# Kernel optimization log

Measured on AMD Instinct MI355X. Metric: run time of the kernel, lower is better.

The kernel has to match this reference:

```python
import jax, jax.numpy as jnp
import numpy as np
from jax import lax

# Constants (canonical show-attend-tell values)
ENCODER_DIM = 2048
ATTENTION_DIM = 512
DECODER_DIM = 512
EMBED_DIM = 512
VOCAB = 10000
B, L, T = 64, 196, 32


def setup_inputs() -> dict:
    key = jax.random.key(0)
    ks = jax.random.split(key, 20)
    s = 0.02
    inp = {
        "encoder_out": jax.random.normal(ks[0], (B, L, ENCODER_DIM), jnp.float32),
        "captions": jax.random.randint(ks[1], (B, T), 0, VOCAB),
        "lengths": jax.random.randint(ks[2], (B,), 2, T + 1).at[0].set(T),
        # parameters (stored as [in, out] for x @ W)
        "emb_table": jax.random.normal(ks[3], (VOCAB, EMBED_DIM), jnp.float32) * s,
        "W_a": jax.random.normal(ks[4], (ENCODER_DIM, ATTENTION_DIM), jnp.float32) * s,
        "U_a": jax.random.normal(ks[5], (DECODER_DIM, ATTENTION_DIM), jnp.float32) * s,
        "w_att": jax.random.normal(ks[6], (ATTENTION_DIM,), jnp.float32) * s,
        "fb_W": jax.random.normal(ks[7], (DECODER_DIM, 1), jnp.float32) * s,
        "fb_b": jnp.zeros((1,), jnp.float32),
        "W_ih": jax.random.normal(ks[8], (4 * DECODER_DIM, EMBED_DIM + ENCODER_DIM), jnp.float32) * s,
        "W_hh": jax.random.normal(ks[9], (4 * DECODER_DIM, DECODER_DIM), jnp.float32) * s,
        "b_ih": jnp.zeros((4 * DECODER_DIM,), jnp.float32),
        "b_hh": jnp.zeros((4 * DECODER_DIM,), jnp.float32),
        "fc_W": jax.random.normal(ks[10], (DECODER_DIM, VOCAB), jnp.float32) * s,
        "fc_b": jnp.zeros((VOCAB,), jnp.float32),
        "ih_W": jax.random.normal(ks[11], (ENCODER_DIM, DECODER_DIM), jnp.float32) * s,
        "ih_b": jnp.zeros((DECODER_DIM,), jnp.float32),
        "ic_W": jax.random.normal(ks[12], (ENCODER_DIM, DECODER_DIM), jnp.float32) * s,
        "ic_b": jnp.zeros((DECODER_DIM,), jnp.float32),
    }
    return inp


def reference(encoder_out, captions, lengths, emb_table, W_a, U_a, w_att,
              fb_W, fb_b, W_ih, W_hh, b_ih, b_hh, fc_W, fc_b,
              ih_W, ih_b, ic_W, ic_b):
    # sort by descending length (as in original)
    sort_idx = jnp.argsort(-lengths)
    enc = encoder_out[sort_idx]          # [B, L, D_enc]
    caps = captions[sort_idx]            # [B, T]
    dl = lengths[sort_idx] - 1           # decode lengths, max == T-1 by construction
    max_t = caps.shape[1] - 1

    emb = emb_table[caps]                # [B, T, E]
    mean = enc.mean(axis=1)
    h0 = jnp.tanh(mean @ ih_W + ih_b)    # [B, H]
    c0 = jnp.tanh(mean @ ic_W + ic_b)

    Wa_enc = enc @ W_a                   # [B, L, A], precomputed once

    def step(carry, xs):
        h, c = carry
        e_t, mask = xs                   # [B, E], [B] bool (dl > t)
        att = jnp.tanh(Wa_enc + (h @ U_a)[:, None, :])        # [B, L, A]
        energy = jnp.einsum('bla,a->bl', att, w_att)          # [B, L]
        alpha = jax.nn.softmax(energy, axis=1)
        context = jnp.einsum('bl,ble->be', alpha, enc)        # [B, D_enc]
        beta = jax.nn.sigmoid(h @ fb_W + fb_b)                # [B, 1]
        context = beta * context
        x = jnp.concatenate([e_t, context], axis=1)           # [B, E+D_enc]
        gates = x @ W_ih.T + b_ih + h @ W_hh.T + b_hh         # [B, 4H]
        i, f, g, o = jnp.split(gates, 4, axis=1)
        i = jax.nn.sigmoid(i); f = jax.nn.sigmoid(f)
        g = jnp.tanh(g); o = jax.nn.sigmoid(o)
        c_new = f * c + i * g
        h_new = o * jnp.tanh(c_new)
        m = mask[:, None]
        h2 = jnp.where(m, h_new, h)
        c2 = jnp.where(m, c_new, c)
        pred = jnp.where(m, h_new @ fc_W + fc_b, 0.0)         # [B, V]
        a_out = jnp.where(m, alpha, 0.0)
        return (h2, c2), (pred, a_out)

    xs = (emb[:, :max_t].transpose(1, 0, 2),                  # [T-1, B, E]
          jnp.arange(max_t)[:, None] < dl[None, :])           # [T-1, B]
    _, (preds, alphas) = lax.scan(step, (h0, c0), xs)
    predictions = preds.transpose(1, 0, 2)                    # [B, T-1, V]
    alphas = alphas.transpose(1, 0, 2)                        # [B, T-1, L]
    return predictions, caps, dl, alphas, sort_idx
```

## Files before the change

### kernel.cpp

```cpp
#include <hip/hip_runtime.h>
#include <cstdint>
#include <cstddef>

#define BB 64
#define LL 196
#define EE 2048
#define AD 512
#define DD 512
#define EM 512
#define VV 10000
#define TTOK 32
#define MT 31
#define KX 3072
#define G4 2048
#define VPAD 10048

#define OUT_PRED 0
#define OUT_CAPS (BB*MT*VV)
#define OUT_DL   (OUT_CAPS + BB*TTOK)
#define OUT_ALPH (OUT_DL + BB)
#define OUT_SIDX (OUT_ALPH + BB*MT*LL)

#define OFF_SIDX 0
#define OFF_DL   64
#define OFF_MEAN 128
#define OFF_C    (OFF_MEAN + BB*EE)
#define OFF_HU   (OFF_C + BB*DD)
#define OFF_ATT  (OFF_HU + BB*AD)
#define OFF_GACC (OFF_ATT + BB*256)
#define OFF_HB   (OFF_GACC + BB*G4)
#define OFF_XFB  (OFF_HB + BB*DD/2)
#define OFF_WB   (OFF_XFB + BB*KX/2)
#define OFF_FCWB (OFF_WB + (size_t)G4*KX/2)
#define OFF_UAB  (OFF_FCWB + (size_t)VPAD*DD/2)
#define OFF_WAB  (OFF_UAB + (size_t)AD*DD/2)
#define OFF_WAEB (OFF_WAB + (size_t)AD*EE/2)
#define OFF_EBF  (OFF_WAEB + (size_t)BB*LL*AD/2)
#define OFF_MEANB OFF_WAEB
#define OFF_IHB  (OFF_WAEB + 65536)
#define OFF_ICB  (OFF_WAEB + 65536 + 524288)

typedef unsigned short u16;
typedef __attribute__((ext_vector_type(8))) short bf16x8;
typedef __attribute__((ext_vector_type(4))) float f32x4;
#define MFMA16(a,b,c) __builtin_amdgcn_mfma_f32_16x16x32_bf16(a,b,c,0,0,0)

__device__ inline u16 f2bf(float x){
    unsigned u = __float_as_uint(x);
    unsigned r = (u + 0x7FFFu + ((u >> 16) & 1u)) >> 16;
    return (u16)r;
}
__device__ inline float bf2f(u16 x){ return __uint_as_float(((unsigned)x) << 16); }
__device__ inline float sigm(float x){ return 1.0f/(1.0f + __expf(-x)); }
__device__ inline float ftanh(float x){ return 2.0f/(1.0f + __expf(-2.0f*x)) - 1.0f; }

__device__ inline void gload16(const u16* g, u16* l){
    __builtin_amdgcn_global_load_lds((const __attribute__((address_space(1))) void*)g,
                                     (__attribute__((address_space(3))) void*)l, 16, 0, 0);
}

__global__ void k_sort(const int* __restrict__ lengths, const int* __restrict__ captions,
                       float* __restrict__ out, int* __restrict__ sidx, int* __restrict__ dl){
    __shared__ int len_s[BB];
    __shared__ int pos_s[BB];
    int i = threadIdx.x;
    len_s[i] = lengths[i];
    __syncthreads();
    int li = len_s[i];
    int rank = 0;
    for (int j = 0; j < BB; j++){
        int lj = len_s[j];
        rank += (lj > li) || (lj == li && j < i);
    }
    pos_s[rank] = i;
    __syncthreads();
    int src = pos_s[i];
    sidx[i] = src;
    int d = len_s[src] - 1;
    dl[i] = d;
    out[OUT_SIDX + i] = (float)src;
    out[OUT_DL + i]   = (float)d;
    for (int t = 0; t < TTOK; t++)
        out[OUT_CAPS + i*TTOK + t] = (float)captions[src*TTOK + t];
}

__global__ void k_ginit(float* __restrict__ gacc, float* __restrict__ mean){
    int gid = blockIdx.x*256 + threadIdx.x;
    if (gid < 65536) gacc[gid] = 0.f;
    else mean[gid - 65536] = 0.f;
}

__global__ void k_meanbf(const float* __restrict__ enc, const int* __restrict__ sidx,
                         float* __restrict__ mean, u16* __restrict__ ebf){
    int b = blockIdx.y;
    int e = (blockIdx.x*256 + threadIdx.x)*4;
    int l0 = blockIdx.z*98, l1 = l0 + 98;
    int src = sidx[b];
    const float* p = enc + (size_t)src*LL*EE + e;
    u16* o = ebf + (size_t)b*LL*EE + e;
    float sx = 0.f, sy = 0.f, sz = 0.f, sw = 0.f;
    for (int l = l0; l < l1; l++){
        float4 v = *(const float4*)(p + (size_t)l*EE);
        sx += v.x; sy += v.y; sz += v.z; sw += v.w;
        unsigned lo = (unsigned)f2bf(v.x) | ((unsigned)f2bf(v.y) << 16);
        unsigned hi = (unsigned)f2bf(v.z) | ((unsigned)f2bf(v.w) << 16);
        uint2 pk; pk.x = lo; pk.y = hi;
        *(uint2*)(o + (size_t)l*EE) = pk;
    }
    atomicAdd(&mean[b*EE + e + 0], sx);
    atomicAdd(&mean[b*EE + e + 1], sy);
    atomicAdd(&mean[b*EE + e + 2], sz);
    atomicAdd(&mean[b*EE + e + 3], sw);
}

__global__ void k_meanb(const float* __restrict__ mean, u16* __restrict__ meanb){
    int i = (blockIdx.x*256 + threadIdx.x)*8;
    float4 a = *(const float4*)(mean + i);
    float4 b = *(const float4*)(mean + i + 4);
// ... 43 lines not shown
    f32x4 acc[4] = {zz,zz,zz,zz};
    #pragma unroll 4
    for (int kc = 0; kc < 16; kc++){
        bf16x8 bv = *(const bf16x8*)(bp + kc*32);
        bf16x8 a0 = *(const bf16x8*)(ap + kc*32);
        bf16x8 a1 = *(const bf16x8*)(ap + 16*EE + kc*32);
        bf16x8 a2 = *(const bf16x8*)(ap + 32*EE + kc*32);
        bf16x8 a3 = *(const bf16x8*)(ap + 48*EE + kc*32);
        acc[0] = MFMA16(a0, bv, acc[0]);
        acc[1] = MFMA16(a1, bv, acc[1]);
        acc[2] = MFMA16(a2, bv, acc[2]);
        acc[3] = MFMA16(a3, bv, acc[3]);
    }
    int j = n0 + lane15;
    #pragma unroll
    for (int mt = 0; mt < 4; mt++)
        #pragma unroll
        for (int r = 0; r < 4; r++){
            int m = mt*16 + quad*4 + r;
            atomicAdd(&hc[z*32768 + m*512 + j], acc[mt][r]);
        }
}

__global__ void k_h0c0f(float* __restrict__ gacc, const float* __restrict__ ih_b,
                        const float* __restrict__ ic_b, const float* __restrict__ b_ih,
                        const float* __restrict__ b_hh, u16* __restrict__ hb,
                        float* __restrict__ c, u16* __restrict__ xfb){
    int gid = blockIdx.x*256 + threadIdx.x;
    if (gid < 65536){
        int z = gid >> 15;
        int mj = gid & 32767;
        int m = mj >> 9, j = mj & 511;
        float v = tanhf(gacc[gid] + (z ? ic_b[j] : ih_b[j]));
        if (z == 0){
            u16 hv = f2bf(v);
            hb[m*DD + j] = hv;
            xfb[(size_t)m*KX + 2560 + j] = hv;
        } else {
            c[m*DD + j] = v;
        }
    }
    int jj = gid & (G4-1);
    gacc[gid] = b_ih[jj] + b_hh[jj];
}

#define BKK 64
__global__ __launch_bounds__(256) void k_waenc2(const u16* __restrict__ ebf,
                                                const u16* __restrict__ Wab,
                                                u16* __restrict__ Waeb){
    __shared__ __align__(16) u16 As[2][128*BKK];
    __shared__ __align__(16) u16 Bs[2][128*BKK];
    int tid = threadIdx.x, lane = tid & 63, w = tid >> 6;
    int lane15 = lane & 15, quad = lane >> 4;
    int m0 = blockIdx.x * 128;
    int n0 = blockIdx.y * 128;

    int srow = w*8 + (lane >> 3);
    int scol = 8 * ((lane & 7) ^ (lane >> 3));
    const u16* ag = ebf + (size_t)(m0 + srow)*EE + scol;
    const u16* bg = Wab + (size_t)(n0 + srow)*EE + scol;

    f32x4 zz = {0.f,0.f,0.f,0.f};
    f32x4 acc[4][4];
    #pragma unroll
    for (int mt = 0; mt < 4; mt++)
        #pragma unroll
        for (int nt = 0; nt < 4; nt++) acc[mt][nt] = zz;

    int ar  = (w >> 1) * 64;
    int brr = (w & 1) * 64;
    int rx  = (lane15 & 7) << 3;

    {
        u16* la = &As[0][w*512 + lane*8];
        u16* lb = &Bs[0][w*512 + lane*8];
        #pragma unroll
        for (int i = 0; i < 4; i++){
            gload16(ag + (size_t)(i*32)*EE, la + i*2048);
            gload16(bg + (size_t)(i*32)*EE, lb + i*2048);
        }
    }
    __syncthreads();

    int cur = 0;
    for (int kt = 0; kt < 32; kt++){
        if (kt < 31){
            u16* la = &As[cur^1][w*512 + lane*8];
            u16* lb = &Bs[cur^1][w*512 + lane*8];
            const u16* a = ag + (size_t)(kt+1)*BKK;
            const u16* b = bg + (size_t)(kt+1)*BKK;
            #pragma unroll
            for (int i = 0; i < 4; i++){
                gload16(a + (size_t)(i*32)*EE, la + i*2048);
                gload16(b + (size_t)(i*32)*EE, lb + i*2048);
            }
        }
        bf16x8 af[4][2], bfr[4][2];
        #pragma unroll
        for (int mt = 0; mt < 4; mt++)
            #pragma unroll
            for (int ks = 0; ks < 2; ks++){
                af[mt][ks]  = *(const bf16x8*)&As[cur][(ar  + mt*16 + lane15)*BKK + ((ks*32 + quad*8) ^ rx)];
                bfr[mt][ks] = *(const bf16x8*)&Bs[cur][(brr + mt*16 + lane15)*BKK + ((ks*32 + quad*8) ^ rx)];
            }
        #pragma unroll
        for (int ks = 0; ks < 2; ks++)
            #pragma unroll
            for (int mt = 0; mt < 4; mt++)
                #pragma unroll
                for (int nt = 0; nt < 4; nt++)
                    acc[mt][nt] = MFMA16(af[mt][ks], bfr[nt][ks], acc[mt][nt]);
        __syncthreads();
        cur ^= 1;
    }

    #pragma unroll
    for (int mt = 0; mt < 4; mt++)
        #pragma unroll
        for (int nt = 0; nt < 4; nt++)
            #pragma unroll
            for (int r = 0; r < 4; r++){
                int row = m0 + ar + mt*16 + quad*4 + r;
                Waeb[(size_t)row*AD + n0 + brr + nt*16 + lane15] = f2bf(acc[mt][nt][r]);
            }
}

__global__ __launch_bounds__(256) void k_energyA(const u16* __restrict__ Waeb,
                       const float* __restrict__ hU, const float* __restrict__ w_att,
                       float* __restrict__ en){
    int tid = threadIdx.x, lane = tid & 63, w = tid >> 6;
    int b = blockIdx.x >> 2, sub = blockIdx.x & 3;

    const float* hub = hU + (size_t)b*AD;
    float hw[8], ww[8];
    #pragma unroll
    for (int ii = 0; ii < 8; ii++){
        hw[ii] = hub[ii*64 + lane];
        ww[ii] = w_att[ii*64 + lane];
    }
    int l0 = sub*49;
    for (int l = l0 + w; l < l0 + 49; l += 4){
        const u16* wa = Waeb + ((size_t)b*LL + l)*AD;
        float acc = 0.f;
        #pragma unroll
        for (int ii = 0; ii < 8; ii++)
            acc += ftanh(bf2f(wa[ii*64 + lane]) + hw[ii]) * ww[ii];
        #pragma unroll
        for (int off = 32; off; off >>= 1) acc += __shfl_xor(acc, off, 64);
        if (lane == 0) en[b*256 + l] = acc;
    }
}

__global__ __launch_bounds__(256) void k_ctx(const float* __restrict__ en,
                      const u16* __restrict__ ebf, const u16* __restrict__ hb,
                      const float* __restrict__ fb_W, const float* __restrict__ fb_b,
                      const float* __restrict__ emb_table, const int* __restrict__ captions,
                      const int* __restrict__ sidx, const int* __restrict__ dl,
                      u16* __restrict__ xfb, float* __restrict__ out, int t){
    __shared__ float red[256];
    __shared__ float alpha_s[LL];
    __shared__ float sbeta;
    int b = blockIdx.y, q = blockIdx.x, tid = threadIdx.x;

    float e = (tid < LL) ? en[b*256 + tid] : -3.0e38f;
    red[tid] = e; __syncthreads();
    for (int s = 128; s > 0; s >>= 1){ if (tid < s) red[tid] = fmaxf(red[tid], red[tid+s]); __syncthreads(); }
    float mx = red[0]; __syncthreads();
    float p = (tid < LL) ? __expf(e - mx) : 0.f;
    red[tid] = p; __syncthreads();
    for (int s = 128; s > 0; s >>= 1){ if (tid < s) red[tid] += red[tid+s]; __syncthreads(); }
    float ssum = red[0]; __syncthreads();
    float alpha = p / ssum;
    if (tid < LL){
        alpha_s[tid] = alpha;
        if (q == 0)
            out[OUT_ALPH + ((size_t)b*MT + t)*LL + tid] = (t < dl[b]) ? alpha : 0.f;
    }

    red[tid] = bf2f(hb[b*DD + tid]) * fb_W[tid]
             + bf2f(hb[b*DD + 256 + tid]) * fb_W[256 + tid];
    __syncthreads();
    for (int s = 128; s > 0; s >>= 1){ if (tid < s) red[tid] += red[tid+s]; __syncthreads(); }
    if (tid == 0) sbeta = sigm(red[0] + fb_b[0]);

    int cap = captions[sidx[b]*TTOK + t];
    if (tid < 128)
        xfb[(size_t)b*KX + q*128 + tid] = f2bf(emb_table[(size_t)cap*EM + q*128 + tid]);
    __syncthreads();

    float beta = sbeta;
    int e0 = q*512 + tid*2;
    const u16* pe = ebf + (size_t)b*LL*EE + e0;
    float ax = 0.f, ay = 0.f;
    for (int l = 0; l < LL; l++){
        unsigned u = *(const unsigned*)(pe + (size_t)l*EE);
        float a = alpha_s[l];
        ax += a * __uint_as_float(u << 16);
        ay += a * __uint_as_float(u & 0xFFFF0000u);
    }
    unsigned pk = (unsigned)f2bf(beta*ax) | ((unsigned)f2bf(beta*ay) << 16);
    *(unsigned*)(xfb + (size_t)b*KX + EM + e0) = pk;
}

__global__ void k_gates(const u16* __restrict__ Wb, const u16* __restrict__ xfb,
                        float* __restrict__ gacc){
    int tid = threadIdx.x, lane = tid & 63, w = tid >> 6;
    int lane15 = lane & 15, quad = lane >> 4;
    int n0 = blockIdx.x*64 + w*16;
    int kbase = blockIdx.y*384;
    const u16* bp = Wb + (size_t)(n0 + lane15)*KX + kbase + quad*8;
    const u16* ap = xfb + (size_t)lane15*KX + kbase + quad*8;
    f32x4 z = {0.f,0.f,0.f,0.f};
    f32x4 acc[4] = {z,z,z,z};
    #pragma unroll 4
    for (int kc = 0; kc < 12; kc++){
        bf16x8 bv = *(const bf16x8*)(bp + kc*32);
        bf16x8 a0 = *(const bf16x8*)(ap + kc*32);
        bf16x8 a1 = *(const bf16x8*)(ap + 16*KX + kc*32);
        bf16x8 a2 = *(const bf16x8*)(ap + 32*KX + kc*32);
        bf16x8 a3 = *(const bf16x8*)(ap + 48*KX + kc*32);
        acc[0] = MFMA16(a0, bv, acc[0]);
        acc[1] = MFMA16(a1, bv, acc[1]);
        acc[2] = MFMA16(a2, bv, acc[2]);
        acc[3] = MFMA16(a3, bv, acc[3]);
    }
    #pragma unroll
    for (int mt = 0; mt < 4; mt++)
        #pragma unroll
        for (int r = 0; r < 4; r++){
            int m = mt*16 + quad*4 + r;
            atomicAdd(&gacc[(size_t)m*G4 + n0 + lane15], acc[mt][r]);
        }
}

__global__ void k_update(float* __restrict__ gacc, const float* __restrict__ b_ih,
                         const float* __restrict__ b_hh, const int* __restrict__ dl,
                         u16* __restrict__ hb, float* __restrict__ c,
                         u16* __restrict__ xfb, int t){
    int gid = blockIdx.x*256 + threadIdx.x;
    int b = gid >> 9, d = gid & 511;
    size_t base = (size_t)b*G4 + d;
    float gi = gacc[base];
    float gf = gacc[base + 512];
    float gg = gacc[base + 1024];
    float go = gacc[base + 1536];
    float ig = sigm(gi), fg = sigm(gf), g = ftanh(gg), o = sigm(go);
    float cold = c[gid];
    float cn = fg*cold + ig*g;
    float hn = o*ftanh(cn);
    if (t < dl[b]){
        c[gid] = cn;
        u16 hv = f2bf(hn);
        hb[gid] = hv;
        xfb[(size_t)b*KX + 2560 + d] = hv;
    }
    gacc[base]        = b_ih[d]        + b_hh[d];
    gacc[base + 512]  = b_ih[d + 512]  + b_hh[d + 512];
    gacc[base + 1024] = b_ih[d + 1024] + b_hh[d + 1024];
    gacc[base + 1536] = b_ih[d + 1536] + b_hh[d + 1536];
}

__global__ void k_pred(const u16* __restrict__ fcWb, const float* __restrict__ fc_b,
                       const u16* __restrict__ Uab, const u16* __restrict__ hb,
                       const int* __restrict__ dl, float* __restrict__ out,
                       float* __restrict__ hU, int t, int hu_only){
    int tid = threadIdx.x, lane = tid & 63, w = tid >> 6;
    int lane15 = lane & 15, quad = lane >> 4;
    int bid = blockIdx.x;
    bool pred; int jc;
    if (hu_only){ pred = false; jc = bid; }
    else if (bid < 157){ pred = true; jc = bid; }
    else { pred = false; jc = bid - 157; }
    const u16* W = pred ? fcWb : Uab;
    int n0 = jc*64 + w*16;
    const u16* bp = W + (size_t)(n0 + lane15)*AD + quad*8;
    const u16* ap = hb + (size_t)lane15*AD + quad*8;
    f32x4 z = {0.f,0.f,0.f,0.f};
    f32x4 acc[4] = {z,z,z,z};
    #pragma unroll 4
    for (int kc = 0; kc < 16; kc++){
        bf16x8 bv = *(const bf16x8*)(bp + kc*32);
        bf16x8 a0 = *(const bf16x8*)(ap + kc*32);
        bf16x8 a1 = *(const bf16x8*)(ap + 16*AD + kc*32);
        bf16x8 a2 = *(const bf16x8*)(ap + 32*AD + kc*32);
        bf16x8 a3 = *(const bf16x8*)(ap + 48*AD + kc*32);
        acc[0] = MFMA16(a0, bv, acc[0]);
        acc[1] = MFMA16(a1, bv, acc[1]);
        acc[2] = MFMA16(a2, bv, acc[2]);
        acc[3] = MFMA16(a3, bv, acc[3]);
    }
    if (pred){
        int j = n0 + lane15;
        if (j < VV){
            float bias = fc_b[j];
            #pragma unroll
            for (int mt = 0; mt < 4; mt++)
                #pragma unroll
                for (int r = 0; r < 4; r++){
                    int b = mt*16 + quad*4 + r;
                    bool mk = t < dl[b];
                    out[OUT_PRED + ((size_t)b*MT + t)*VV + j] = mk ? acc[mt][r] + bias : 0.f;
                }
        }
    } else {
        int n = n0 + lane15;
        #pragma unroll
        for (int mt = 0; mt < 4; mt++)
            #pragma unroll
            for (int r = 0; r < 4; r++){
                int b = mt*16 + quad*4 + r;
                hU[(size_t)b*AD + n] = acc[mt][r];
            }
    }
}

extern "C" void kernel_launch(void* const* d_in, const int* in_sizes, int n_in,
                              void* d_out, int out_size, void* d_ws, size_t ws_size,
                              hipStream_t stream) {
    const float* enc       = (const float*)d_in[0];
    const int*   captions  = (const int*)d_in[1];
    const int*   lengths   = (const int*)d_in[2];
    const float* emb_table = (const float*)d_in[3];
    const float* W_a       = (const float*)d_in[4];
    const float* U_a       = (const float*)d_in[5];
    const float* w_att     = (const float*)d_in[6];
    const float* fb_W      = (const float*)d_in[7];
    const float* fb_b      = (const float*)d_in[8];
    const float* W_ih      = (const float*)d_in[9];
    const float* W_hh      = (const float*)d_in[10];
    const float* b_ih      = (const float*)d_in[11];
    const float* b_hh      = (const float*)d_in[12];
    const float* fc_W      = (const float*)d_in[13];
    const float* fc_b      = (const float*)d_in[14];
    const float* ih_W      = (const float*)d_in[15];
    const float* ih_b      = (const float*)d_in[16];
    const float* ic_W      = (const float*)d_in[17];
    const float* ic_b      = (const float*)d_in[18];

    float* out = (float*)d_out;
    float* ws  = (float*)d_ws;
    int* sidx = (int*)(ws + OFF_SIDX);
    int* dl   = (int*)(ws + OFF_DL);
    float* mean = ws + OFF_MEAN;
    float* c    = ws + OFF_C;
    float* hU   = ws + OFF_HU;
    float* en   = ws + OFF_ATT;
    float* gacc = ws + OFF_GACC;
    u16* hb   = (u16*)(ws + OFF_HB);
    u16* xfb  = (u16*)(ws + OFF_XFB);
    u16* Wb   = (u16*)(ws + OFF_WB);
    u16* fcWb = (u16*)(ws + OFF_FCWB);
    u16* Uab  = (u16*)(ws + OFF_UAB);
    u16* Wab  = (u16*)(ws + OFF_WAB);
    u16* Waeb = (u16*)(ws + OFF_WAEB);
    u16* ebf  = (u16*)(ws + OFF_EBF);
    u16* meanb = (u16*)(ws + OFF_MEANB);
    u16* ihb  = (u16*)(ws + OFF_IHB);
    u16* icb  = (u16*)(ws + OFF_ICB);

    k_sort<<<1, 64, 0, stream>>>(lengths, captions, out, sidx, dl);
    k_ginit<<<768, 256, 0, stream>>>(gacc, mean);
    k_meanbf<<<dim3(2, BB, 2), 256, 0, stream>>>(enc, sidx, mean, ebf);
    k_meanb<<<64, 256, 0, stream>>>(mean, meanb);
    k_tr<<<dim3(64, 16), dim3(32, 8), 0, stream>>>(ih_W, ihb, 2048, 512);
    k_tr<<<dim3(64, 16), dim3(32, 8), 0, stream>>>(ic_W, icb, 2048, 512);
    k_h0c0s<<<dim3(8, 2, 4), 256, 0, stream>>>(ihb, icb, meanb, gacc);
    k_h0c0f<<<512, 256, 0, stream>>>(gacc, ih_b, ic_b, b_ih, b_hh, hb, c, xfb);
    k_wb<<<dim3(12, G4), 256, 0, stream>>>(W_ih, W_hh, Wb);
    k_tr<<<dim3(16, 314), dim3(32, 8), 0, stream>>>(fc_W, fcWb, 512, VV);
    k_tr<<<dim3(16, 16),  dim3(32, 8), 0, stream>>>(U_a, Uab, 512, 512);
    k_tr<<<dim3(64, 16),  dim3(32, 8), 0, stream>>>(W_a, Wab, 2048, 512);
    k_waenc2<<<dim3(98, 4), 256, 0, stream>>>(ebf, Wab, Waeb);
    k_pred<<<8, 256, 0, stream>>>(fcWb, fc_b, Uab, hb, dl, out, hU, 0, 1);

    for (int t = 0; t < MT; t++){
        k_energyA<<<256, 256, 0, stream>>>(Waeb, hU, w_att, en);
        k_ctx<<<dim3(4, BB), 256, 0, stream>>>(en, ebf, hb, fb_W, fb_b,
                                               emb_table, captions, sidx, dl, xfb, out, t);
        k_gates<<<dim3(32, 8), 256, 0, stream>>>(Wb, xfb, gacc);
        k_update<<<128, 256, 0, stream>>>(gacc, b_ih, b_hh, dl, hb, c, xfb, t);
        k_pred<<<165, 256, 0, stream>>>(fcWb, fc_b, Uab, hb, dl, out, hU, t, 0);
    }
}
```

Measured before the change: 2.229 ms.

## Fuse per-timestep decoder kernels into one persistent kernel with grid barriers

Replaces the five kernels launched per timestep (energy, context, gates, update, prediction) with a single persistent kernel of 128 blocks of 512 threads that loops over all timesteps. Phases are separated by a software grid barrier built on atomic counters kept in workspace and reset in k_sort. This removes about 155 kernel launches and their gaps, at the cost of fewer blocks per phase (for example, the vocab projection now runs on 83 blocks instead of 165), spin-wait barrier overhead, and reliance on all 128 blocks being co-resident. The waenc GEMM grid is also transposed so consecutive blocks cover the N dimension.

```diff
diff --git a/kernel.cpp b/kernel.cpp
--- a/kernel.cpp
+++ b/kernel.cpp
@@ -14,6 +14,7 @@
 #define KX 3072
 #define G4 2048
 #define VPAD 10048
+#define NBLK 128
 
 #define OUT_PRED 0
 #define OUT_CAPS (BB*MT*VV)
@@ -59,11 +60,30 @@
                                      (__attribute__((address_space(3))) void*)l, 16, 0, 0);
 }
 
+__device__ inline void gbar(int* cnt, int* gen){
+    __syncthreads();
+    if (threadIdx.x == 0){
+        __threadfence();
+        int g = __hip_atomic_load(gen, __ATOMIC_RELAXED, __HIP_MEMORY_SCOPE_AGENT);
+        if (__hip_atomic_fetch_add(cnt, 1, __ATOMIC_ACQ_REL, __HIP_MEMORY_SCOPE_AGENT) == NBLK-1){
+            __hip_atomic_store(cnt, 0, __ATOMIC_RELAXED, __HIP_MEMORY_SCOPE_AGENT);
+            __hip_atomic_fetch_add(gen, 1, __ATOMIC_RELEASE, __HIP_MEMORY_SCOPE_AGENT);
+        } else {
+            while (__hip_atomic_load(gen, __ATOMIC_RELAXED, __HIP_MEMORY_SCOPE_AGENT) == g)
+                __builtin_amdgcn_s_sleep(2);
+        }
+        __threadfence();
+    }
+    __syncthreads();
+}
+
 __global__ void k_sort(const int* __restrict__ lengths, const int* __restrict__ captions,
-                       float* __restrict__ out, int* __restrict__ sidx, int* __restrict__ dl){
+                       float* __restrict__ out, int* __restrict__ sidx, int* __restrict__ dl,
+                       int* __restrict__ bar){
     __shared__ int len_s[BB];
     __shared__ int pos_s[BB];
     int i = threadIdx.x;
+    if (i < 2) bar[i] = 0;
     len_s[i] = lengths[i];
     __syncthreads();
     int li = len_s[i];
@@ -213,8 +233,8 @@
     __shared__ __align__(16) u16 Bs[2][128*BKK];
     int tid = threadIdx.x, lane = tid & 63, w = tid >> 6;
     int lane15 = lane & 15, quad = lane >> 4;
-    int m0 = blockIdx.x * 128;
-    int n0 = blockIdx.y * 128;
+    int m0 = blockIdx.y * 128;
+    int n0 = blockIdx.x * 128;
 
     int srow = w*8 + (lane >> 3);
     int scol = 8 * ((lane & 7) ^ (lane >> 3));
@@ -286,155 +306,198 @@
             }
 }
 
-__global__ __launch_bounds__(256) void k_energyA(const u16* __restrict__ Waeb,
-                       const float* __restrict__ hU, const float* __restrict__ w_att,
-                       float* __restrict__ en){
-    int tid = threadIdx.x, lane = tid & 63, w = tid >> 6;
-    int b = blockIdx.x >> 2, sub = blockIdx.x & 3;
-
-    const float* hub = hU + (size_t)b*AD;
-    float hw[8], ww[8];
-    #pragma unroll
-    for (int ii = 0; ii < 8; ii++){
-        hw[ii] = hub[ii*64 + lane];
-        ww[ii] = w_att[ii*64 + lane];
-    }
-    int l0 = sub*49;
-    for (int l = l0 + w; l < l0 + 49; l += 4){
-        const u16* wa = Waeb + ((size_t)b*LL + l)*AD;
-        float acc = 0.f;
-        #pragma unroll
-        for (int ii = 0; ii < 8; ii++)
-            acc += ftanh(bf2f(wa[ii*64 + lane]) + hw[ii]) * ww[ii];
-        #pragma unroll
-        for (int off = 32; off; off >>= 1) acc += __shfl_xor(acc, off, 64);
-        if (lane == 0) en[b*256 + l] = acc;
-    }
-}
-
-__global__ __launch_bounds__(256) void k_ctx(const float* __restrict__ en,
-                      const u16* __restrict__ ebf, const u16* __restrict__ hb,
-                      const float* __restrict__ fb_W, const float* __restrict__ fb_b,
-                      const float* __restrict__ emb_table, const int* __restrict__ captions,
-                      const int* __restrict__ sidx, const int* __restrict__ dl,
-                      u16* __restrict__ xfb, float* __restrict__ out, int t){
-    __shared__ float red[256];
+__global__ __launch_bounds__(512) void k_loop(
+    const u16* __restrict__ Waeb, float* __restrict__ hU, u16* __restrict__ hb,
+    const float* __restrict__ w_att, const float* __restrict__ fb_W,
+    const float* __restrict__ fb_b, const float* __restrict__ emb_table,
+    const int* __restrict__ captions, const int* __restrict__ sidx,
+    const int* __restrict__ dl, const u16* __restrict__ ebf,
+    u16* __restrict__ xfb, float* __restrict__ en, float* __restrict__ gacc,
+    const u16* __restrict__ Wb, const float* __restrict__ b_ih,
+    const float* __restrict__ b_hh, float* __restrict__ c,
+    const u16* __restrict__ fcWb, const float* __restrict__ fc_b,
+    const u16* __restrict__ Uab, float* __restrict__ out, int* bar)
+{
+    __shared__ float red[512];
     __shared__ float alpha_s[LL];
     __shared__ float sbeta;
-    int b = blockIdx.y, q = blockIdx.x, tid = threadIdx.x;
-
-    float e = (tid < LL) ? en[b*256 + tid] : -3.0e38f;
-    red[tid] = e; __syncthreads();
-    for (int s = 128; s > 0; s >>= 1){ if (tid < s) red[tid] = fmaxf(red[tid], red[tid+s]); __syncthreads(); }
-    float mx = red[0]; __syncthreads();
-    float p = (tid < LL) ? __expf(e - mx) : 0.f;
-    red[tid] = p; __syncthreads();
-    for (int s = 128; s > 0; s >>= 1){ if (tid < s) red[tid] += red[tid+s]; __syncthreads(); }
-    float ssum = red[0]; __syncthreads();
-    float alpha = p / ssum;
-    if (tid < LL){
-        alpha_s[tid] = alpha;
-        if (q == 0)
-            out[OUT_ALPH + ((size_t)b*MT + t)*LL + tid] = (t < dl[b]) ? alpha : 0.f;
-    }
-
-    red[tid] = bf2f(hb[b*DD + tid]) * fb_W[tid]
-             + bf2f(hb[b*DD + 256 + tid]) * fb_W[256 + tid];
-    __syncthreads();
-    for (int s = 128; s > 0; s >>= 1){ if (tid < s) red[tid] += red[tid+s]; __syncthreads(); }
-    if (tid == 0) sbeta = sigm(red[0] + fb_b[0]);
-
-    int cap = captions[sidx[b]*TTOK + t];
-    if (tid < 128)
-        xfb[(size_t)b*KX + q*128 + tid] = f2bf(emb_table[(size_t)cap*EM + q*128 + tid]);
-    __syncthreads();
-
-    float beta = sbeta;
-    int e0 = q*512 + tid*2;
-    const u16* pe = ebf + (size_t)b*LL*EE + e0;
-    float ax = 0.f, ay = 0.f;
-    for (int l = 0; l < LL; l++){
-        unsigned u = *(const unsigned*)(pe + (size_t)l*EE);
-        float a = alpha_s[l];
-        ax += a * __uint_as_float(u << 16);
-        ay += a * __uint_as_float(u & 0xFFFF0000u);
-    }
-    unsigned pk = (unsigned)f2bf(beta*ax) | ((unsigned)f2bf(beta*ay) << 16);
-    *(unsigned*)(xfb + (size_t)b*KX + EM + e0) = pk;
-}
-
-__global__ void k_gates(const u16* __restrict__ Wb, const u16* __restrict__ xfb,
-                        float* __restrict__ gacc){
+    int bid = blockIdx.x, tid = threadIdx.x;
+    int lane = tid & 63, w = tid >> 6;
+    int lane15 = lane & 15, quad = lane >> 4;
+    int* cnt = bar;
+    int* gen = bar + 1;
+
+    for (int t = 0; t < MT; t++){
+        {
+            int b = bid >> 1, sub = bid & 1;
+            int cap = captions[sidx[b]*TTOK + t];
+            if (tid < 256)
+                xfb[(size_t)b*KX + sub*256 + tid] = f2bf(emb_table[(size_t)cap*EM + sub*256 + tid]);
+            const float* hub = hU + (size_t)b*AD;
+            float hw[8], ww[8];
+            #pragma unroll
+            for (int ii = 0; ii < 8; ii++){
+                hw[ii] = hub[ii*64 + lane];
+                ww[ii] = w_att[ii*64 + lane];
+            }
+            int l0 = sub*98;
+            for (int l = l0 + w; l < l0 + 98; l += 8){
+                const u16* wa = Waeb + ((size_t)b*LL + l)*AD;
+                float acc = 0.f;
+                #pragma unroll
+                for (int ii = 0; ii < 8; ii++)
+                    acc += ftanh(bf2f(wa[ii*64 + lane]) + hw[ii]) * ww[ii];
+                #pragma unroll
+                for (int off = 32; off; off >>= 1) acc += __shfl_xor(acc, off, 64);
+                if (lane == 0) en[b*256 + l] = acc;
+            }
+        }
+        gbar(cnt, gen);
+        {
+            int b = bid >> 1, q = bid & 1;
+            float e = (tid < LL) ? en[b*256 + tid] : -3.0e38f;
+            red[tid] = e; __syncthreads();
+            for (int s = 256; s > 0; s >>= 1){ if (tid < s) red[tid] = fmaxf(red[tid], red[tid+s]); __syncthreads(); }
+            float mx = red[0]; __syncthreads();
+            float p = (tid < LL) ? __expf(e - mx) : 0.f;
+            red[tid] = p; __syncthreads();
+            for (int s = 256; s > 0; s >>= 1){ if (tid < s) red[tid] += red[tid+s]; __syncthreads(); }
+            float ssum = red[0]; __syncthreads();
+            float alpha = p / ssum;
+            if (tid < LL){
+                alpha_s[tid] = alpha;
+                if (q == 0)
+                    out[OUT_ALPH + ((size_t)b*MT + t)*LL + tid] = (t < dl[b]) ? alpha : 0.f;
+            }
+            red[tid] = bf2f(hb[b*DD + tid]) * fb_W[tid];
+            __syncthreads();
+            for (int s = 256; s > 0; s >>= 1){ if (tid < s) red[tid] += red[tid+s]; __syncthreads(); }
+            if (tid == 0) sbeta = sigm(red[0] + fb_b[0]);
+            __syncthreads();
+            float beta = sbeta;
+            int e0 = q*1024 + tid*2;
+            const u16* pe = ebf + (size_t)b*LL*EE + e0;
+            float ax = 0.f, ay = 0.f;
+            for (int l = 0; l < LL; l++){
+                unsigned u = *(const unsigned*)(pe + (size_t)l*EE);
+                float a = alpha_s[l];
+                ax += a * __uint_as_float(u << 16);
+                ay += a * __uint_as_float(u & 0xFFFF0000u);
+            }
+            unsigned pk = (unsigned)f2bf(beta*ax) | ((unsigned)f2bf(beta*ay) << 16);
+            *(unsigned*)(xfb + (size_t)b*KX + EM + e0) = pk;
+        }
+        gbar(cnt, gen);
+        {
+            int n0 = (bid & 15)*128 + w*16;
+            int kbase = (bid >> 4)*384;
+            const u16* bp = Wb + (size_t)(n0 + lane15)*KX + kbase + quad*8;
+            const u16* ap = xfb + (size_t)lane15*KX + kbase + quad*8;
+            f32x4 z4 = {0.f,0.f,0.f,0.f};
+            f32x4 acc[4] = {z4,z4,z4,z4};
+            #pragma unroll 4
+            for (int kc = 0; kc < 12; kc++){
+                bf16x8 bv = *(const bf16x8*)(bp + kc*32);
+                bf16x8 a0 = *(const bf16x8*)(ap + kc*32);
+                bf16x8 a1 = *(const bf16x8*)(ap + 16*KX + kc*32);
+                bf16x8 a2 = *(const bf16x8*)(ap + 32*KX + kc*32);
+                bf16x8 a3 = *(const bf16x8*)(ap + 48*KX + kc*32);
+                acc[0] = MFMA16(a0, bv, acc[0]);
+                acc[1] = MFMA16(a1, bv, acc[1]);
+                acc[2] = MFMA16(a2, bv, acc[2]);
+                acc[3] = MFMA16(a3, bv, acc[3]);
+            }
+            #pragma unroll
+            for (int mt = 0; mt < 4; mt++)
+                #pragma unroll
+                for (int r = 0; r < 4; r++){
+                    int m = mt*16 + quad*4 + r;
+                    atomicAdd(&gacc[(size_t)m*G4 + n0 + lane15], acc[mt][r]);
+                }
+        }
+        gbar(cnt, gen);
+        {
+            int gid = bid*512 + tid;
+            if (gid < BB*DD){
+                int b = gid >> 9, d = gid & 511;
+                size_t base = (size_t)b*G4 + d;
+                float gi = gacc[base];
+                float gf = gacc[base + 512];
+                float gg = gacc[base + 1024];
+                float go = gacc[base + 1536];
+                float ig = sigm(gi), fg = sigm(gf), g = ftanh(gg), o = sigm(go);
+                float cold = c[gid];
+                float cn = fg*cold + ig*g;
+                float hn = o*ftanh(cn);
+                if (t < dl[b]){
+                    c[gid] = cn;
+                    u16 hv = f2bf(hn);
+                    hb[gid] = hv;
+                    xfb[(size_t)b*KX + 2560 + d] = hv;
+                }
+                gacc[base]        = b_ih[d]        + b_hh[d];
+                gacc[base + 512]  = b_ih[d + 512]  + b_hh[d + 512];
+                gacc[base + 1024] = b_ih[d + 1024] + b_hh[d + 1024];
+                gacc[base + 1536] = b_ih[d + 1536] + b_hh[d + 1536];
+            }
+        }
+        gbar(cnt, gen);
+        if (bid < 83){
+            bool pred = bid < 79;
+            int n0 = (pred ? bid : (bid - 79))*128 + w*16;
+            const u16* W = pred ? fcWb : Uab;
+            int rowb = n0 + lane15;
+            if (pred && rowb >= VPAD) rowb = 0;
+            const u16* bp = W + (size_t)rowb*AD + quad*8;
+            const u16* ap = hb + (size_t)lane15*AD + quad*8;
+            f32x4 z4 = {0.f,0.f,0.f,0.f};
+            f32x4 acc[4] = {z4,z4,z4,z4};
+            #pragma unroll 4
+            for (int kc = 0; kc < 16; kc++){
+                bf16x8 bv = *(const bf16x8*)(bp + kc*32);
+                bf16x8 a0 = *(const bf16x8*)(ap + kc*32);
+                bf16x8 a1 = *(const bf16x8*)(ap + 16*AD + kc*32);
+                bf16x8 a2 = *(const bf16x8*)(ap + 32*AD + kc*32);
+                bf16x8 a3 = *(const bf16x8*)(ap + 48*AD + kc*32);
+                acc[0] = MFMA16(a0, bv, acc[0]);
+                acc[1] = MFMA16(a1, bv, acc[1]);
+                acc[2] = MFMA16(a2, bv, acc[2]);
+                acc[3] = MFMA16(a3, bv, acc[3]);
+            }
+            if (pred){
+                int j = n0 + lane15;
+                if (j < VV){
+                    float bias = fc_b[j];
+                    #pragma unroll
+                    for (int mt = 0; mt < 4; mt++)
+                        #pragma unroll
+                        for (int r = 0; r < 4; r++){
+                            int b = mt*16 + quad*4 + r;
+                            bool mk = t < dl[b];
+                            out[OUT_PRED + ((size_t)b*MT + t)*VV + j] = mk ? acc[mt][r] + bias : 0.f;
+                        }
+                }
+            } else {
+                int n = n0 + lane15;
+                #pragma unroll
+                for (int mt = 0; mt < 4; mt++)
+                    #pragma unroll
+                    for (int r = 0; r < 4; r++){
+                        int b = mt*16 + quad*4 + r;
+                        hU[(size_t)b*AD + n] = acc[mt][r];
+                    }
+            }
+        }
+        gbar(cnt, gen);
+    }
+}
+
+__global__ void k_pred0(const u16* __restrict__ Uab, const u16* __restrict__ hb,
+                        float* __restrict__ hU){
     int tid = threadIdx.x, lane = tid & 63, w = tid >> 6;
     int lane15 = lane & 15, quad = lane >> 4;
     int n0 = blockIdx.x*64 + w*16;
-    int kbase = blockIdx.y*384;
-    const u16* bp = Wb + (size_t)(n0 + lane15)*KX + kbase + quad*8;
-    const u16* ap = xfb + (size_t)lane15*KX + kbase + quad*8;
-    f32x4 z = {0.f,0.f,0.f,0.f};
-    f32x4 acc[4] = {z,z,z,z};
-    #pragma unroll 4
-    for (int kc = 0; kc < 12; kc++){
-        bf16x8 bv = *(const bf16x8*)(bp + kc*32);
-        bf16x8 a0 = *(const bf16x8*)(ap + kc*32);
-        bf16x8 a1 = *(const bf16x8*)(ap + 16*KX + kc*32);
-        bf16x8 a2 = *(const bf16x8*)(ap + 32*KX + kc*32);
-        bf16x8 a3 = *(const bf16x8*)(ap + 48*KX + kc*32);
-        acc[0] = MFMA16(a0, bv, acc[0]);
-        acc[1] = MFMA16(a1, bv, acc[1]);
-        acc[2] = MFMA16(a2, bv, acc[2]);
-        acc[3] = MFMA16(a3, bv, acc[3]);
-    }
-    #pragma unroll
-    for (int mt = 0; mt < 4; mt++)
-        #pragma unroll
-        for (int r = 0; r < 4; r++){
-            int m = mt*16 + quad*4 + r;
-            atomicAdd(&gacc[(size_t)m*G4 + n0 + lane15], acc[mt][r]);
-        }
-}
-
-__global__ void k_update(float* __restrict__ gacc, const float* __restrict__ b_ih,
-                         const float* __restrict__ b_hh, const int* __restrict__ dl,
-                         u16* __restrict__ hb, float* __restrict__ c,
-                         u16* __restrict__ xfb, int t){
-    int gid = blockIdx.x*256 + threadIdx.x;
-    int b = gid >> 9, d = gid & 511;
-    size_t base = (size_t)b*G4 + d;
-    float gi = gacc[base];
-    float gf = gacc[base + 512];
-    float gg = gacc[base + 1024];
-    float go = gacc[base + 1536];
-    float ig = sigm(gi), fg = sigm(gf), g = ftanh(gg), o = sigm(go);
-    float cold = c[gid];
-    float cn = fg*cold + ig*g;
-    float hn = o*ftanh(cn);
-    if (t < dl[b]){
-        c[gid] = cn;
-        u16 hv = f2bf(hn);
-        hb[gid] = hv;
-        xfb[(size_t)b*KX + 2560 + d] = hv;
-    }
-    gacc[base]        = b_ih[d]        + b_hh[d];
-    gacc[base + 512]  = b_ih[d + 512]  + b_hh[d + 512];
-    gacc[base + 1024] = b_ih[d + 1024] + b_hh[d + 1024];
-    gacc[base + 1536] = b_ih[d + 1536] + b_hh[d + 1536];
-}
-
-__global__ void k_pred(const u16* __restrict__ fcWb, const float* __restrict__ fc_b,
-                       const u16* __restrict__ Uab, const u16* __restrict__ hb,
-                       const int* __restrict__ dl, float* __restrict__ out,
-                       float* __restrict__ hU, int t, int hu_only){
-    int tid = threadIdx.x, lane = tid & 63, w = tid >> 6;
-    int lane15 = lane & 15, quad = lane >> 4;
-    int bid = blockIdx.x;
-    bool pred; int jc;
-    if (hu_only){ pred = false; jc = bid; }
-    else if (bid < 157){ pred = true; jc = bid; }
-    else { pred = false; jc = bid - 157; }
-    const u16* W = pred ? fcWb : Uab;
-    int n0 = jc*64 + w*16;
-    const u16* bp = W + (size_t)(n0 + lane15)*AD + quad*8;
+    const u16* bp = Uab + (size_t)(n0 + lane15)*AD + quad*8;
     const u16* ap = hb + (size_t)lane15*AD + quad*8;
     f32x4 z = {0.f,0.f,0.f,0.f};
     f32x4 acc[4] = {z,z,z,z};
@@ -450,29 +513,14 @@
         acc[2] = MFMA16(a2, bv, acc[2]);
         acc[3] = MFMA16(a3, bv, acc[3]);
     }
-    if (pred){
-        int j = n0 + lane15;
-        if (j < VV){
-            float bias = fc_b[j];
-            #pragma unroll
-            for (int mt = 0; mt < 4; mt++)
-                #pragma unroll
-                for (int r = 0; r < 4; r++){
-                    int b = mt*16 + quad*4 + r;
-                    bool mk = t < dl[b];
-                    out[OUT_PRED + ((size_t)b*MT + t)*VV + j] = mk ? acc[mt][r] + bias : 0.f;
-                }
-        }
-    } else {
-        int n = n0 + lane15;
-        #pragma unroll
-        for (int mt = 0; mt < 4; mt++)
-            #pragma unroll
-            for (int r = 0; r < 4; r++){
-                int b = mt*16 + quad*4 + r;
-                hU[(size_t)b*AD + n] = acc[mt][r];
-            }
-    }
+    int n = n0 + lane15;
+    #pragma unroll
+    for (int mt = 0; mt < 4; mt++)
+        #pragma unroll
+        for (int r = 0; r < 4; r++){
+            int b = mt*16 + quad*4 + r;
+            hU[(size_t)b*AD + n] = acc[mt][r];
+        }
 }
 
 extern "C" void kernel_launch(void* const* d_in, const int* in_sizes, int n_in,
@@ -507,6 +555,7 @@
     float* hU   = ws + OFF_HU;
     float* en   = ws + OFF_ATT;
     float* gacc = ws + OFF_GACC;
+    int* bar  = (int*)(en + BB*256 - 4);
     u16* hb   = (u16*)(ws + OFF_HB);
     u16* xfb  = (u16*)(ws + OFF_XFB);
     u16* Wb   = (u16*)(ws + OFF_WB);
@@ -519,7 +568,7 @@
     u16* ihb  = (u16*)(ws + OFF_IHB);
     u16* icb  = (u16*)(ws + OFF_ICB);
 
-    k_sort<<<1, 64, 0, stream>>>(lengths, captions, out, sidx, dl);
+    k_sort<<<1, 64, 0, stream>>>(lengths, captions, out, sidx, dl, bar);
     k_ginit<<<768, 256, 0, stream>>>(gacc, mean);
     k_meanbf<<<dim3(2, BB, 2), 256, 0, stream>>>(enc, sidx, mean, ebf);
     k_meanb<<<64, 256, 0, stream>>>(mean, meanb);
@@ -531,15 +580,10 @@
     k_tr<<<dim3(16, 314), dim3(32, 8), 0, stream>>>(fc_W, fcWb, 512, VV);
     k_tr<<<dim3(16, 16),  dim3(32, 8), 0, stream>>>(U_a, Uab, 512, 512);
     k_tr<<<dim3(64, 16),  dim3(32, 8), 0, stream>>>(W_a, Wab, 2048, 512);
-    k_waenc2<<<dim3(98, 4), 256, 0, stream>>>(ebf, Wab, Waeb);
-    k_pred<<<8, 256, 0, stream>>>(fcWb, fc_b, Uab, hb, dl, out, hU, 0, 1);
-
-    for (int t = 0; t < MT; t++){
-        k_energyA<<<256, 256, 0, stream>>>(Waeb, hU, w_att, en);
-        k_ctx<<<dim3(4, BB), 256, 0, stream>>>(en, ebf, hb, fb_W, fb_b,
-                                               emb_table, captions, sidx, dl, xfb, out, t);
-        k_gates<<<dim3(32, 8), 256, 0, stream>>>(Wb, xfb, gacc);
-        k_update<<<128, 256, 0, stream>>>(gacc, b_ih, b_hh, dl, hb, c, xfb, t);
-        k_pred<<<165, 256, 0, stream>>>(fcWb, fc_b, Uab, hb, dl, out, hU, t, 0);
-    }
-}
+    k_waenc2<<<dim3(4, 98), 256, 0, stream>>>(ebf, Wab, Waeb);
+    k_pred0<<<8, 256, 0, stream>>>(Uab, hb, hU);
+
+    k_loop<<<NBLK, 512, 0, stream>>>(Waeb, hU, hb, w_att, fb_W, fb_b, emb_table,
+                                     captions, sidx, dl, ebf, xfb, en, gacc, Wb,
+                                     b_ih, b_hh, c, fcWb, fc_b, Uab, out, bar);
+}
```

Result: slower. 4.352 ms (+95.3%).

## Fuse per-step kernels: energy into update, prediction into next-step context

Applied to the files above, without the earlier changes.

The per-timestep loop drops from five kernel launches to three. The attention energy and the hU = h·U_a product are now computed inside the LSTM update kernel, one block per batch row. The vocab prediction for step t-1 runs as extra blocks of the next step's context kernel, with a final launch for the last step. The aim is to cut launch overhead and serialization on the recurrent critical path. The trade-off is that the fused update kernel runs only 64 blocks and does the energy work with low parallelism. The waenc grid axes are also swapped.

```diff
diff --git a/kernel.cpp b/kernel.cpp
--- a/kernel.cpp
+++ b/kernel.cpp
@@ -213,8 +213,8 @@
     __shared__ __align__(16) u16 Bs[2][128*BKK];
     int tid = threadIdx.x, lane = tid & 63, w = tid >> 6;
     int lane15 = lane & 15, quad = lane >> 4;
-    int m0 = blockIdx.x * 128;
-    int n0 = blockIdx.y * 128;
+    int m0 = blockIdx.y * 128;
+    int n0 = blockIdx.x * 128;
 
     int srow = w*8 + (lane >> 3);
     int scol = 8 * ((lane & 7) ^ (lane >> 3));
@@ -286,81 +286,86 @@
             }
 }
 
-__global__ __launch_bounds__(256) void k_energyA(const u16* __restrict__ Waeb,
-                       const float* __restrict__ hU, const float* __restrict__ w_att,
-                       float* __restrict__ en){
-    int tid = threadIdx.x, lane = tid & 63, w = tid >> 6;
-    int b = blockIdx.x >> 2, sub = blockIdx.x & 3;
-
-    const float* hub = hU + (size_t)b*AD;
-    float hw[8], ww[8];
-    #pragma unroll
-    for (int ii = 0; ii < 8; ii++){
-        hw[ii] = hub[ii*64 + lane];
-        ww[ii] = w_att[ii*64 + lane];
-    }
-    int l0 = sub*49;
-    for (int l = l0 + w; l < l0 + 49; l += 4){
-        const u16* wa = Waeb + ((size_t)b*LL + l)*AD;
-        float acc = 0.f;
-        #pragma unroll
-        for (int ii = 0; ii < 8; ii++)
-            acc += ftanh(bf2f(wa[ii*64 + lane]) + hw[ii]) * ww[ii];
-        #pragma unroll
-        for (int off = 32; off; off >>= 1) acc += __shfl_xor(acc, off, 64);
-        if (lane == 0) en[b*256 + l] = acc;
-    }
-}
-
-__global__ __launch_bounds__(256) void k_ctx(const float* __restrict__ en,
+__global__ __launch_bounds__(256) void k_ctxpred(const float* __restrict__ en,
                       const u16* __restrict__ ebf, const u16* __restrict__ hb,
                       const float* __restrict__ fb_W, const float* __restrict__ fb_b,
-                      const float* __restrict__ emb_table, const int* __restrict__ captions,
-                      const int* __restrict__ sidx, const int* __restrict__ dl,
-                      u16* __restrict__ xfb, float* __restrict__ out, int t){
-    __shared__ float red[256];
-    __shared__ float alpha_s[LL];
-    __shared__ float sbeta;
-    int b = blockIdx.y, q = blockIdx.x, tid = threadIdx.x;
-
-    float e = (tid < LL) ? en[b*256 + tid] : -3.0e38f;
-    red[tid] = e; __syncthreads();
-    for (int s = 128; s > 0; s >>= 1){ if (tid < s) red[tid] = fmaxf(red[tid], red[tid+s]); __syncthreads(); }
-    float mx = red[0]; __syncthreads();
-    float p = (tid < LL) ? __expf(e - mx) : 0.f;
-    red[tid] = p; __syncthreads();
-    for (int s = 128; s > 0; s >>= 1){ if (tid < s) red[tid] += red[tid+s]; __syncthreads(); }
-    float ssum = red[0]; __syncthreads();
-    float alpha = p / ssum;
-    if (tid < LL){
-        alpha_s[tid] = alpha;
-        if (q == 0)
-            out[OUT_ALPH + ((size_t)b*MT + t)*LL + tid] = (t < dl[b]) ? alpha : 0.f;
-    }
-
-    red[tid] = bf2f(hb[b*DD + tid]) * fb_W[tid]
-             + bf2f(hb[b*DD + 256 + tid]) * fb_W[256 + tid];
-    __syncthreads();
-    for (int s = 128; s > 0; s >>= 1){ if (tid < s) red[tid] += red[tid+s]; __syncthreads(); }
-    if (tid == 0) sbeta = sigm(red[0] + fb_b[0]);
-
-    int cap = captions[sidx[b]*TTOK + t];
-    if (tid < 128)
-        xfb[(size_t)b*KX + q*128 + tid] = f2bf(emb_table[(size_t)cap*EM + q*128 + tid]);
-    __syncthreads();
-
-    float beta = sbeta;
-    int e0 = q*512 + tid*2;
-    const u16* pe = ebf + (size_t)b*LL*EE + e0;
-    float ax = 0.f, ay = 0.f;
-    for (int l = 0; l < LL; l++){
-        unsigned u = *(const unsigned*)(pe + (size_t)l*EE);
-        float a = alpha_s[l];
-        ax += a * __uint_as_float(u << 16);
-        ay += a * __uint_as_float(u & 0xFFFF0000u);
-    }
-    unsigned pk = (unsigned)f2bf(beta*ax) | ((unsigned)f2bf(beta*ay) << 16);
-    *(unsigned*)(xfb + (size_t)b*KX + EM + e0) = pk;
+                      const u16* __restrict__ fcWb, const float* __restrict__ fc_b,
+                      const int* __restrict__ dl, u16* __restrict__ xfb,
+                      float* __restrict__ out, int t, int mode){
+    int bid = blockIdx.x, tid = threadIdx.x;
+    if (mode == 0 && bid < 256){
+        __shared__ float red[256];
+        __shared__ float alpha_s[LL];
+        __shared__ float sbeta;
+        int b = bid >> 2, q = bid & 3;
+        float e = (tid < LL) ? en[b*256 + tid] : -3.0e38f;
+        red[tid] = e; __syncthreads();
+        for (int s = 128; s > 0; s >>= 1){ if (tid < s) red[tid] = fmaxf(red[tid], red[tid+s]); __syncthreads(); }
+        float mx = red[0]; __syncthreads();
+        float p = (tid < LL) ? __expf(e - mx) : 0.f;
+        red[tid] = p; __syncthreads();
+        for (int s = 128; s > 0; s >>= 1){ if (tid < s) red[tid] += red[tid+s]; __syncthreads(); }
+        float ssum = red[0]; __syncthreads();
+        float alpha = p / ssum;
+        if (tid < LL){
+            alpha_s[tid] = alpha;
+            if (q == 0)
+                out[OUT_ALPH + ((size_t)b*MT + t)*LL + tid] = (t < dl[b]) ? alpha : 0.f;
+        }
+        red[tid] = bf2f(hb[b*DD + tid]) * fb_W[tid]
+                 + bf2f(hb[b*DD + 256 + tid]) * fb_W[256 + tid];
+        __syncthreads();
+        for (int s = 128; s > 0; s >>= 1){ if (tid < s) red[tid] += red[tid+s]; __syncthreads(); }
+        if (tid == 0) sbeta = sigm(red[0] + fb_b[0]);
+        __syncthreads();
+        float beta = sbeta;
+        int e0 = q*512 + tid*2;
+        const u16* pe = ebf + (size_t)b*LL*EE + e0;
+        float ax = 0.f, ay = 0.f;
+        for (int l = 0; l < LL; l++){
+            unsigned u = *(const unsigned*)(pe + (size_t)l*EE);
+            float a = alpha_s[l];
+            ax += a * __uint_as_float(u << 16);
+            ay += a * __uint_as_float(u & 0xFFFF0000u);
+        }
+        unsigned pk = (unsigned)f2bf(beta*ax) | ((unsigned)f2bf(beta*ay) << 16);
+        *(unsigned*)(xfb + (size_t)b*KX + EM + e0) = pk;
+        return;
+    }
+    if (mode == 0 && t == 0) return;
+    int jc = (mode == 0) ? bid - 256 : bid;
+    int tp = (mode == 0) ? t - 1 : MT - 1;
+    int lane = tid & 63, w = tid >> 6;
+    int lane15 = lane & 15, quad = lane >> 4;
+    int n0 = jc*64 + w*16;
+    const u16* bp = fcWb + (size_t)(n0 + lane15)*AD + quad*8;
+    const u16* ap = hb + (size_t)lane15*AD + quad*8;
+    f32x4 z = {0.f,0.f,0.f,0.f};
+    f32x4 acc[4] = {z,z,z,z};
+    #pragma unroll 4
+    for (int kc = 0; kc < 16; kc++){
+        bf16x8 bv = *(const bf16x8*)(bp + kc*32);
+        bf16x8 a0 = *(const bf16x8*)(ap + kc*32);
+        bf16x8 a1 = *(const bf16x8*)(ap + 16*AD + kc*32);
+        bf16x8 a2 = *(const bf16x8*)(ap + 32*AD + kc*32);
+        bf16x8 a3 = *(const bf16x8*)(ap + 48*AD + kc*32);
+        acc[0] = MFMA16(a0, bv, acc[0]);
+        acc[1] = MFMA16(a1, bv, acc[1]);
+        acc[2] = MFMA16(a2, bv, acc[2]);
+        acc[3] = MFMA16(a3, bv, acc[3]);
+    }
+    int j = n0 + lane15;
+    if (j < VV){
+        float bias = fc_b[j];
+        #pragma unroll
+        for (int mt = 0; mt < 4; mt++)
+            #pragma unroll
+            for (int r = 0; r < 4; r++){
+                int b = mt*16 + quad*4 + r;
+                bool mk = tp < dl[b];
+                out[OUT_PRED + ((size_t)b*MT + tp)*VV + j] = mk ? acc[mt][r] + bias : 0.f;
+            }
+    }
 }
 
 __global__ void k_gates(const u16* __restrict__ Wb, const u16* __restrict__ xfb,
@@ -394,84 +399,82 @@
         }
 }
 
-__global__ void k_update(float* __restrict__ gacc, const float* __restrict__ b_ih,
-                         const float* __restrict__ b_hh, const int* __restrict__ dl,
-                         u16* __restrict__ hb, float* __restrict__ c,
-                         u16* __restrict__ xfb, int t){
-    int gid = blockIdx.x*256 + threadIdx.x;
-    int b = gid >> 9, d = gid & 511;
-    size_t base = (size_t)b*G4 + d;
-    float gi = gacc[base];
-    float gf = gacc[base + 512];
-    float gg = gacc[base + 1024];
-    float go = gacc[base + 1536];
-    float ig = sigm(gi), fg = sigm(gf), g = ftanh(gg), o = sigm(go);
-    float cold = c[gid];
-    float cn = fg*cold + ig*g;
-    float hn = o*ftanh(cn);
-    if (t < dl[b]){
-        c[gid] = cn;
-        u16 hv = f2bf(hn);
-        hb[gid] = hv;
-        xfb[(size_t)b*KX + 2560 + d] = hv;
-    }
-    gacc[base]        = b_ih[d]        + b_hh[d];
-    gacc[base + 512]  = b_ih[d + 512]  + b_hh[d + 512];
-    gacc[base + 1024] = b_ih[d + 1024] + b_hh[d + 1024];
-    gacc[base + 1536] = b_ih[d + 1536] + b_hh[d + 1536];
-}
-
-__global__ void k_pred(const u16* __restrict__ fcWb, const float* __restrict__ fc_b,
-                       const u16* __restrict__ Uab, const u16* __restrict__ hb,
-                       const int* __restrict__ dl, float* __restrict__ out,
-                       float* __restrict__ hU, int t, int hu_only){
-    int tid = threadIdx.x, lane = tid & 63, w = tid >> 6;
-    int lane15 = lane & 15, quad = lane >> 4;
-    int bid = blockIdx.x;
-    bool pred; int jc;
-    if (hu_only){ pred = false; jc = bid; }
-    else if (bid < 157){ pred = true; jc = bid; }
-    else { pred = false; jc = bid - 157; }
-    const u16* W = pred ? fcWb : Uab;
-    int n0 = jc*64 + w*16;
-    const u16* bp = W + (size_t)(n0 + lane15)*AD + quad*8;
-    const u16* ap = hb + (size_t)lane15*AD + quad*8;
-    f32x4 z = {0.f,0.f,0.f,0.f};
-    f32x4 acc[4] = {z,z,z,z};
-    #pragma unroll 4
-    for (int kc = 0; kc < 16; kc++){
-        bf16x8 bv = *(const bf16x8*)(bp + kc*32);
-        bf16x8 a0 = *(const bf16x8*)(ap + kc*32);
-        bf16x8 a1 = *(const bf16x8*)(ap + 16*AD + kc*32);
-        bf16x8 a2 = *(const bf16x8*)(ap + 32*AD + kc*32);
-        bf16x8 a3 = *(const bf16x8*)(ap + 48*AD + kc*32);
-        acc[0] = MFMA16(a0, bv, acc[0]);
-        acc[1] = MFMA16(a1, bv, acc[1]);
-        acc[2] = MFMA16(a2, bv, acc[2]);
-        acc[3] = MFMA16(a3, bv, acc[3]);
-    }
-    if (pred){
-        int j = n0 + lane15;
-        if (j < VV){
-            float bias = fc_b[j];
+__global__ __launch_bounds__(512) void k_update(float* __restrict__ gacc,
+                         const float* __restrict__ b_ih, const float* __restrict__ b_hh,
+                         const int* __restrict__ dl, u16* __restrict__ hb,
+                         float* __restrict__ c, u16* __restrict__ xfb,
+                         const u16* __restrict__ Uab, const u16* __restrict__ Waeb,
+                         const float* __restrict__ w_att, float* __restrict__ en,
+                         const float* __restrict__ emb_table, const int* __restrict__ captions,
+                         const int* __restrict__ sidx, int t){
+    __shared__ float hs[DD];
+    __shared__ float hu_s[AD];
+    int b = blockIdx.x, tid = threadIdx.x;
+    int lane = tid & 63, w = tid >> 6;
+
+    if (t >= 0){
+        int d = tid;
+        size_t base = (size_t)b*G4 + d;
+        float gi = gacc[base];
+        float gf = gacc[base + 512];
+        float gg = gacc[base + 1024];
+        float go = gacc[base + 1536];
+        float ig = sigm(gi), fg = sigm(gf), g = ftanh(gg), o = sigm(go);
+        int gid = b*DD + d;
+        float cold = c[gid];
+        float cn = fg*cold + ig*g;
+        float hn = o*ftanh(cn);
+        bool mk = t < dl[b];
+        float h2 = mk ? hn : bf2f(hb[gid]);
+        hs[d] = h2;
+        if (mk){
+            c[gid] = cn;
+            u16 hv = f2bf(h2);
+            hb[gid] = hv;
+            xfb[(size_t)b*KX + 2560 + d] = hv;
+        }
+        gacc[base]        = b_ih[d]        + b_hh[d];
+        gacc[base + 512]  = b_ih[d + 512]  + b_hh[d + 512];
+        gacc[base + 1024] = b_ih[d + 1024] + b_hh[d + 1024];
+        gacc[base + 1536] = b_ih[d + 1536] + b_hh[d + 1536];
+    } else {
+        hs[tid] = bf2f(hb[b*DD + tid]);
+    }
+    __syncthreads();
+    if (t == MT-1) return;
+
+    int cap = captions[sidx[b]*TTOK + (t+1)];
+    xfb[(size_t)b*KX + tid] = f2bf(emb_table[(size_t)cap*EM + tid]);
+
+    {
+        const u16* up = Uab + (size_t)tid*AD;
+        float acc = 0.f;
+        #pragma unroll 8
+        for (int d = 0; d < DD; d += 8){
+            bf16x8 uv = *(const bf16x8*)(up + d);
             #pragma unroll
-            for (int mt = 0; mt < 4; mt++)
-                #pragma unroll
-                for (int r = 0; r < 4; r++){
-                    int b = mt*16 + quad*4 + r;
-                    bool mk = t < dl[b];
-                    out[OUT_PRED + ((size_t)b*MT + t)*VV + j] = mk ? acc[mt][r] + bias : 0.f;
-                }
-        }
-    } else {
-        int n = n0 + lane15;
-        #pragma unroll
-        for (int mt = 0; mt < 4; mt++)
-            #pragma unroll
-            for (int r = 0; r < 4; r++){
-                int b = mt*16 + quad*4 + r;
-                hU[(size_t)b*AD + n] = acc[mt][r];
-            }
+            for (int j2 = 0; j2 < 8; j2++)
+                acc += bf2f((u16)uv[j2]) * hs[d + j2];
+        }
+        hu_s[tid] = acc;
+    }
+    __syncthreads();
+
+    float hw[8], ww[8];
+    #pragma unroll
+    for (int ii = 0; ii < 8; ii++){
+        hw[ii] = hu_s[ii*64 + lane];
+        ww[ii] = w_att[ii*64 + lane];
+    }
+    for (int l = w; l < LL; l += 8){
+        const u16* wa = Waeb + ((size_t)b*LL + l)*AD;
+        float acc = 0.f;
+        #pragma unroll
+        for (int ii = 0; ii < 8; ii++)
+            acc += ftanh(bf2f(wa[ii*64 + lane]) + hw[ii]) * ww[ii];
+        #pragma unroll
+        for (int off = 32; off; off >>= 1) acc += __shfl_xor(acc, off, 64);
+        if (lane == 0) en[b*256 + l] = acc;
     }
 }
 
@@ -504,7 +507,6 @@
     int* dl   = (int*)(ws + OFF_DL);
     float* mean = ws + OFF_MEAN;
     float* c    = ws + OFF_C;
-    float* hU   = ws + OFF_HU;
     float* en   = ws + OFF_ATT;
     float* gacc = ws + OFF_GACC;
     u16* hb   = (u16*)(ws + OFF_HB);
@@ -531,15 +533,17 @@
     k_tr<<<dim3(16, 314), dim3(32, 8), 0, stream>>>(fc_W, fcWb, 512, VV);
     k_tr<<<dim3(16, 16),  dim3(32, 8), 0, stream>>>(U_a, Uab, 512, 512);
     k_tr<<<dim3(64, 16),  dim3(32, 8), 0, stream>>>(W_a, Wab, 2048, 512);
-    k_waenc2<<<dim3(98, 4), 256, 0, stream>>>(ebf, Wab, Waeb);
-    k_pred<<<8, 256, 0, stream>>>(fcWb, fc_b, Uab, hb, dl, out, hU, 0, 1);
+    k_waenc2<<<dim3(4, 98), 256, 0, stream>>>(ebf, Wab, Waeb);
+    k_update<<<64, 512, 0, stream>>>(gacc, b_ih, b_hh, dl, hb, c, xfb, Uab, Waeb,
+                                     w_att, en, emb_table, captions, sidx, -1);
 
     for (int t = 0; t < MT; t++){
-        k_energyA<<<256, 256, 0, stream>>>(Waeb, hU, w_att, en);
-        k_ctx<<<dim3(4, BB), 256, 0, stream>>>(en, ebf, hb, fb_W, fb_b,
-                                               emb_table, captions, sidx, dl, xfb, out, t);
+        k_ctxpred<<<413, 256, 0, stream>>>(en, ebf, hb, fb_W, fb_b, fcWb, fc_b,
+                                           dl, xfb, out, t, 0);
         k_gates<<<dim3(32, 8), 256, 0, stream>>>(Wb, xfb, gacc);
-        k_update<<<128, 256, 0, stream>>>(gacc, b_ih, b_hh, dl, hb, c, xfb, t);
-        k_pred<<<165, 256, 0, stream>>>(fcWb, fc_b, Uab, hb, dl, out, hU, t, 0);
-    }
-}
+        k_update<<<64, 512, 0, stream>>>(gacc, b_ih, b_hh, dl, hb, c, xfb, Uab, Waeb,
+                                         w_att, en, emb_table, captions, sidx, t);
+    }
+    k_ctxpred<<<157, 256, 0, stream>>>(en, ebf, hb, fb_W, fb_b, fcWb, fc_b,
+                                       dl, xfb, out, MT, 1);
+}
```

After: 2.568 ms. +15.2%, slower.
